# Kernel optimization log

Hardware: AMD Instinct MI355X
Metric: run time of the kernel (lower is better)

## Reference

```python
import jax, jax.numpy as jnp
import numpy as np

N = 50000
E = 800000
IN_DIM = 128
EMB_DIM = 64
HID = 128
OUT_DIM = 64
VOCAB = 1000
NUM_GRAPHS = 128


def _gat(x, src, dst, W, a_s, a_d, b, n):
    # PyG GATConv, heads=1: h = x @ W (no bias); alpha_e = leaky_relu(a_s.h_src + a_d.h_dst, 0.2)
    h = x @ W                                  # [n, C]
    as_n = h @ a_s                             # [n]
    ad_n = h @ a_d                             # [n]
    logit = jax.nn.leaky_relu(as_n[src] + ad_n[dst], negative_slope=0.2)  # [E']
    # segment softmax over destination node
    m = jax.ops.segment_max(logit, dst, num_segments=n)
    e = jnp.exp(logit - m[dst])
    s = jax.ops.segment_sum(e, dst, num_segments=n)
    coef = e / s[dst]                          # [E']
    out = jax.ops.segment_sum(h[src] * coef[:, None], dst, num_segments=n)
    return out + b


def setup_inputs() -> dict:
    key = jax.random.key(0)
    ks = jax.random.split(key, 20)
    inp = {
        "x": jax.random.normal(ks[0], (N, IN_DIM), dtype=jnp.float32),
        "node_index": jax.random.randint(ks[1], (N,), 0, VOCAB),
        "edge_index": jax.random.randint(ks[2], (2, E), 0, N),
        "batch": jnp.sort(jax.random.randint(ks[3], (N,), 0, NUM_GRAPHS)),
        "emb": jax.random.normal(ks[4], (VOCAB, EMB_DIM), dtype=jnp.float32) * 0.1,
        "W1": jax.random.normal(ks[5], (IN_DIM + EMB_DIM, HID), dtype=jnp.float32) * 0.05,
        "a1s": jax.random.normal(ks[6], (HID,), dtype=jnp.float32) * 0.1,
        "a1d": jax.random.normal(ks[7], (HID,), dtype=jnp.float32) * 0.1,
        "b1": jnp.zeros((HID,), dtype=jnp.float32),
        "W2": jax.random.normal(ks[8], (HID, HID), dtype=jnp.float32) * 0.05,
        "a2s": jax.random.normal(ks[9], (HID,), dtype=jnp.float32) * 0.1,
        "a2d": jax.random.normal(ks[10], (HID,), dtype=jnp.float32) * 0.1,
        "b2": jnp.zeros((HID,), dtype=jnp.float32),
        "W3": jax.random.normal(ks[11], (HID, HID), dtype=jnp.float32) * 0.05,
        "a3s": jax.random.normal(ks[12], (HID,), dtype=jnp.float32) * 0.1,
        "a3d": jax.random.normal(ks[13], (HID,), dtype=jnp.float32) * 0.1,
        "b3": jnp.zeros((HID,), dtype=jnp.float32),
        "fcW": jax.random.normal(ks[14], (HID, OUT_DIM), dtype=jnp.float32) * 0.05,
        "fcb": jnp.zeros((OUT_DIM,), dtype=jnp.float32),
    }
    return inp


def reference(x, node_index, edge_index, batch, emb, W1, a1s, a1d, b1,
              W2, a2s, a2d, b2, W3, a3s, a3d, b3, fcW, fcb):
    n = x.shape[0]
    # embedding lookup + L2 normalize features, then concat
    ev = emb[node_index]                       # [N, EMB_DIM]
    norms = jnp.linalg.norm(x, axis=1, keepdims=True)
    norms = jnp.where(norms == 0, 1e-8, norms)
    h = jnp.concatenate([x / norms, ev], axis=1)  # [N, IN+EMB]
    # add self loops (PyG GATConv default add_self_loops=True)
    loop = jnp.arange(n)
    src = jnp.concatenate([edge_index[0], loop])
    dst = jnp.concatenate([edge_index[1], loop])
    h = jax.nn.gelu(_gat(h, src, dst, W1, a1s, a1d, b1, n))
    h = jax.nn.gelu(_gat(h, src, dst, W2, a2s, a2d, b2, n))
    h = jax.nn.gelu(_gat(h, src, dst, W3, a3s, a3d, b3, n))
    # global_add_pool over graphs
    g = jax.ops.segment_sum(h, batch, num_segments=NUM_GRAPHS)  # [G, HID]
    out = g @ fcW + fcb
    return jax.nn.leaky_relu(out, negative_slope=0.01)
```

## Files before the change

kernel.cpp:

```cpp
#include <hip/hip_runtime.h>

#define N_NODES 50000
#define N_EDGES 800000
#define IN_DIM 128
#define EMB_DIM 64
#define HID 128
#define OUT_DIM 64
#define NUM_GRAPHS 128
#define E_TOT (N_EDGES + N_NODES)
#define K1 (IN_DIM + EMB_DIM)
#define BSH 8
#define BNODES 256
#define NB 196
#define EPT 16
#define EPB (256 * EPT)
#define PREPA_BLOCKS 12500
#define BHIST_BLOCKS 512
#define PB_CAP 5376

typedef __attribute__((ext_vector_type(8))) short bf16x8;
typedef __attribute__((ext_vector_type(4))) float f32x4;

__device__ __forceinline__ float gelu_f(float x) {
    float x3 = x * x * x;
    return 0.5f * x * (1.0f + tanhf(0.7978845608028654f * (x + 0.044715f * x3)));
}
__device__ __forceinline__ float lrelu02(float x) { return x > 0.f ? x : 0.2f * x; }
__device__ __forceinline__ unsigned short f2bf(float f) {
    unsigned u = __float_as_uint(f);
    unsigned r = (u + 0x7fffu + ((u >> 16) & 1u)) >> 16;
    return (unsigned short)r;
}
__device__ __forceinline__ unsigned pk2bf(float a, float b) {
    return (unsigned)f2bf(a) | ((unsigned)f2bf(b) << 16);
}

__global__ __launch_bounds__(128) void k_prepW3(const float* __restrict__ W1, unsigned short* __restrict__ Wt1,
                                                const float* __restrict__ W2, unsigned short* __restrict__ Wt2,
                                                const float* __restrict__ W3, unsigned short* __restrict__ Wt3,
                                                int* __restrict__ bcnt, int* __restrict__ bfill) {
    int b = blockIdx.x;
    int c = threadIdx.x;
    if (b == K1 + 2 * HID) {
        for (int i = c; i < NB; i += 128) { bcnt[i] = 0; bfill[i] = 0; }
        return;
    }
    if (b < K1) {
        Wt1[(size_t)c * (K1 + 8) + b] = f2bf(W1[(size_t)b * HID + c]);
    } else if (b < K1 + HID) {
        int k = b - K1;
        Wt2[(size_t)c * (HID + 8) + k] = f2bf(W2[(size_t)k * HID + c]);
    } else {
        int k = b - K1 - HID;
        Wt3[(size_t)c * (HID + 8) + k] = f2bf(W3[(size_t)k * HID + c]);
    }
}

__global__ __launch_bounds__(256) void k_prepA_bhist(const float* __restrict__ x, const int* __restrict__ nidx,
                                                     const float* __restrict__ emb, unsigned* __restrict__ Abu,
                                                     const int* __restrict__ dst, int* __restrict__ bcnt) {
    __shared__ int h[NB];
    if (blockIdx.x >= PREPA_BLOCKS) {
        int nb = blockIdx.x - PREPA_BLOCKS;
        for (int i = threadIdx.x; i < NB; i += 256) h[i] = 0;
        __syncthreads();
        for (int e = nb * 256 + threadIdx.x; e < N_EDGES; e += BHIST_BLOCKS * 256)
            atomicAdd(&h[dst[e] >> BSH], 1);
        __syncthreads();
        for (int i = threadIdx.x; i < NB; i += 256)
            if (h[i]) atomicAdd(&bcnt[i], h[i]);
        return;
    }
    int lane = threadIdx.x & 63;
    int node = (blockIdx.x * 256 + threadIdx.x) >> 6;
    if (node >= N_NODES) return;
    float2 v = ((const float2*)(x + (size_t)node * IN_DIM))[lane];
    float ss = v.x * v.x + v.y * v.y;
#pragma unroll
    for (int o = 32; o; o >>= 1) ss += __shfl_xor(ss, o);
    float nrm = sqrtf(ss);
    if (nrm == 0.f) nrm = 1e-8f;
    float inv = 1.f / nrm;
    unsigned* row = Abu + (size_t)node * (K1 / 2);
    row[lane] = pk2bf(v.x * inv, v.y * inv);
    int nid = __builtin_amdgcn_readfirstlane(nidx[node]);
    if (lane < 32) {
        float2 e = ((const float2*)(emb + (size_t)nid * EMB_DIM))[lane];
        row[64 + lane] = pk2bf(e.x, e.y);
    }
}

__global__ __launch_bounds__(512) void k_bscan(const int* __restrict__ bcnt, int* __restrict__ boff,
                                               int* __restrict__ rowptr) {
    __shared__ int sh[512];
    int t = threadIdx.x;
    int v = (t < NB) ? bcnt[t] : 0;
    sh[t] = v;
    __syncthreads();
    for (int o = 1; o < 512; o <<= 1) {
        int u = (t >= o) ? sh[t - o] : 0;
        __syncthreads();
        sh[t] += u;
        __syncthreads();
    }
    if (t < NB) boff[t] = sh[t] - v;
    if (t == NB - 1) boff[NB] = sh[t];
    if (t == 0) rowptr[N_NODES] = E_TOT;
}

__global__ __launch_bounds__(256) void k_passA(const int* __restrict__ src, const int* __restrict__ dst,
                                               const int* __restrict__ boff, int* __restrict__ bfill,
                                               unsigned* __restrict__ barr) {
    __shared__ int h[NB];
    __shared__ int hbase[NB];
    __shared__ int lofs[NB];
    __shared__ int ssc[256];
    __shared__ unsigned val[EPB];
    __shared__ unsigned char bid[EPB];
    int t = threadIdx.x;
    for (int i = t; i < NB; i += 256) h[i] = 0;
    __syncthreads();
    int e0 = blockIdx.x * EPB;
    int tag[EPT];
#pragma unroll
    for (int i = 0; i < EPT; i++) {
        int e = e0 + i * 256 + t;
        tag[i] = -1;
        if (e < N_EDGES) {
            int b = dst[e] >> BSH;
            int r = atomicAdd(&h[b], 1);
            tag[i] = (b << 12) | r;
        }
    }
    __syncthreads();
    int v = (t < NB) ? h[t] : 0;
    ssc[t] = v;
    __syncthreads();
    for (int o = 1; o < 256; o <<= 1) {
        int u = (t >= o) ? ssc[t - o] : 0;
        __syncthreads();
        ssc[t] += u;
        __syncthreads();
    }
    if (t < NB) {
        lofs[t] = ssc[t] - v;
        hbase[t] = v ? atomicAdd(&bfill[t], v) : 0;
    }
    __syncthreads();
    int tot = ssc[255];
#pragma unroll
    for (int i = 0; i < EPT; i++) {
        if (tag[i] >= 0) {
            int e = e0 + i * 256 + t;
            int b = tag[i] >> 12, r = tag[i] & 0xfff;
            unsigned s = (unsigned)src[e];
            unsigned dl = (unsigned)(dst[e] & (BNODES - 1));
            int idx = lofs[b] + r;
            val[idx] = s | (dl << 16);
            bid[idx] = (unsigned char)b;
        }
    }
    __syncthreads();
    for (int i = t; i < tot; i += 256) {
        int b = bid[i];
        barr[boff[b] + hbase[b] + (i - lofs[b])] = val[i];
    }
}

__global__ __launch_bounds__(256) void k_passB(const unsigned* __restrict__ barr, const int* __restrict__ boff,
                                               int* __restrict__ rowptr, int* __restrict__ csr) {
    __shared__ int dcnt[256];
    __shared__ int dsum[256];
    __shared__ int locOff[256];
    __shared__ unsigned stg[PB_CAP];
    int b = blockIdx.x;
    int t = threadIdx.x;
    int n0 = b << BSH;
    int cnt = min(BNODES, N_NODES - n0);
    int eb = boff[b], ee = boff[b + 1];
    int ne = ee - eb;
    dcnt[t] = 0;
    __syncthreads();
    for (int i = eb + t; i < ee; i += 256) atomicAdd(&dcnt[barr[i] >> 16], 1);
    __syncthreads();
    int v = (t < cnt) ? dcnt[t] + 1 : 0;
    dsum[t] = v;
    __syncthreads();
    for (int o = 1; o < 256; o <<= 1) {
        int u = (t >= o) ? dsum[t - o] : 0;
        __syncthreads();
        dsum[t] += u;
        __syncthreads();
    }
    int csrBase = eb + n0;
    locOff[t] = dsum[t] - v;
    dcnt[t] = 0;
    if (t < cnt) rowptr[n0 + t] = csrBase + locOff[t];
    int total = ne + cnt;
    __syncthreads();
    if (total <= PB_CAP) {
        if (t < cnt) stg[locOff[t]] = (unsigned)(n0 + t);
        for (int i = eb + t; i < ee; i += 256) {
            unsigned vv = barr[i];
            int dl = vv >> 16;
            int k = atomicAdd(&dcnt[dl], 1);
            stg[locOff[dl] + 1 + k] = vv & 0xffffu;
        }
        __syncthreads();
        for (int i = t; i < total; i += 256) csr[csrBase + i] = (int)stg[i];
    } else {
        if (t < cnt) csr[csrBase + locOff[t]] = n0 + t;
        for (int i = eb + t; i < ee; i += 256) {
            unsigned vv = barr[i];
            int dl = vv >> 16;
            int k = atomicAdd(&dcnt[dl], 1);
            csr[csrBase + locOff[dl] + 1 + k] = (int)(vv & 0xffffu);
        }
    }
}

template <int K>
__global__ __launch_bounds__(256) void k_mgemm(const unsigned short* __restrict__ Abf,
                                               const unsigned short* __restrict__ WtP,
                                               const float* __restrict__ a_s, const float* __restrict__ a_d,
                                               unsigned short* __restrict__ Hbf,
                                               float* __restrict__ asn, float* __restrict__ adn) {
    constexpr int KP = K + 8;
    constexpr int NK = K / 32;
    __shared__ __align__(16) unsigned short Wl[128 * KP];
    {
        const uint4* gsrc = (const uint4*)WtP;
        uint4* ldst = (uint4*)Wl;
        const int nchunk = 128 * KP * 2 / 16;
        for (int i = threadIdx.x; i < nchunk; i += 256) ldst[i] = gsrc[i];
    }
    int lane = threadIdx.x & 63;
    int wv = threadIdx.x >> 6;
    int rowbase = blockIdx.x * 64 + wv * 16;
    if (rowbase >= N_NODES) { __syncthreads(); return; }
    int l15 = lane & 15, quad = lane >> 4;

    const unsigned short* Abase = Abf + (size_t)(rowbase + l15) * K + quad * 8;
    bf16x8 afr[NK];
#pragma unroll
    for (int i = 0; i < NK; i++) afr[i] = *(const bf16x8*)(Abase + i * 32);

    __syncthreads();

    f32x4 acc[8];
#pragma unroll
    for (int t = 0; t < 8; t++) acc[t] = (f32x4){0.f, 0.f, 0.f, 0.f};
#pragma unroll
    for (int i = 0; i < NK; i++) {
#pragma unroll
        for (int t = 0; t < 8; t++) {
            bf16x8 bf = *(const bf16x8*)(&Wl[(t * 16 + l15) * KP + i * 32 + quad * 8]);
            acc[t] = __builtin_amdgcn_mfma_f32_16x16x32_bf16(afr[i], bf, acc[t], 0, 0, 0);
        }
    }
    float asc[8], adc[8];
#pragma unroll
    for (int t = 0; t < 8; t++) { asc[t] = a_s[t * 16 + l15]; adc[t] = a_d[t * 16 + l15]; }
#pragma unroll
    for (int r = 0; r < 4; r++) {
        int row = rowbase + quad * 4 + r;
        float ps = 0.f, pd = 0.f;
#pragma unroll
        for (int t = 0; t < 8; t++) {
            float v = acc[t][r];
            Hbf[(size_t)row * HID + t * 16 + l15] = f2bf(v);
            ps = fmaf(v, asc[t], ps);
            pd = fmaf(v, adc[t], pd);
        }
#pragma unroll
        for (int o = 1; o < 16; o <<= 1) {
            ps += __shfl_xor(ps, o);
            pd += __shfl_xor(pd, o);
        }
        if (l15 == 0) { asn[row] = ps; adn[row] = pd; }
    }
}

template <bool OUT32>
__global__ __launch_bounds__(256) void k_aggr(const int* __restrict__ rowptr, const int* __restrict__ csr,
                                              const float* __restrict__ asn, const float* __restrict__ adn,
                                              const unsigned short* __restrict__ hbf,
                                              const float* __restrict__ bias, void* __restrict__ outp) {
    __shared__ float sh_e[4][64];
    __shared__ int sh_s[4][64];
    int lane = threadIdx.x & 63;
    int w = threadIdx.x >> 6;
    int node = blockIdx.x * 4 + w;
    if (node >= N_NODES) return;
    int st = rowptr[node], en = rowptr[node + 1];
    int deg = en - st;
    float ad = adn[node];

    if (deg <= 64) {
        int s = 0;
        float l = -1e30f;
        if (lane < deg) {
            s = csr[st + lane];
            l = lrelu02(asn[s] + ad);
        }
        float m = l;
#pragma unroll
        for (int o = 32; o; o >>= 1) m = fmaxf(m, __shfl_xor(m, o));
        float e = (lane < deg) ? __expf(l - m) : 0.f;
        float ssum = e;
#pragma unroll
        for (int o = 32; o; o >>= 1) ssum += __shfl_xor(ssum, o);
        float coef = e / ssum;

        const uint2* hu2 = (const uint2*)hbf;
        int half = lane >> 5, li = lane & 31;
        float4 acc = make_float4(0.f, 0.f, 0.f, 0.f);
        int j = 0;
        for (; j + 16 <= deg; j += 16) {
            int sx[8];
            float cf[8];
            uint2 vv[8];
#pragma unroll
            for (int q = 0; q < 8; q++) {
                int ii = j + 2 * q + half;
                sx[q] = __shfl(s, ii);
                cf[q] = __shfl(coef, ii);
            }
#pragma unroll
            for (int q = 0; q < 8; q++) vv[q] = hu2[(size_t)sx[q] * 32 + li];
#pragma unroll
            for (int q = 0; q < 8; q++) {
                acc.x = fmaf(cf[q], __int_as_float(vv[q].x << 16), acc.x);
                acc.y = fmaf(cf[q], __int_as_float(vv[q].x & 0xffff0000u), acc.y);
                acc.z = fmaf(cf[q], __int_as_float(vv[q].y << 16), acc.z);
                acc.w = fmaf(cf[q], __int_as_float(vv[q].y & 0xffff0000u), acc.w);
            }
        }
        for (; j + 8 <= deg; j += 8) {
            int sx[4];
            float cf[4];
            uint2 vv[4];
#pragma unroll
            for (int q = 0; q < 4; q++) {
                int ii = j + 2 * q + half;
                sx[q] = __shfl(s, ii);
                cf[q] = __shfl(coef, ii);
            }
#pragma unroll
            for (int q = 0; q < 4; q++) vv[q] = hu2[(size_t)sx[q] * 32 + li];
#pragma unroll
            for (int q = 0; q < 4; q++) {
                acc.x = fmaf(cf[q], __int_as_float(vv[q].x << 16), acc.x);
                acc.y = fmaf(cf[q], __int_as_float(vv[q].x & 0xffff0000u), acc.y);
                acc.z = fmaf(cf[q], __int_as_float(vv[q].y << 16), acc.z);
                acc.w = fmaf(cf[q], __int_as_float(vv[q].y & 0xffff0000u), acc.w);
            }
        }
        for (; j < deg; j += 2) {
            int ii = j + half;
            int ok = ii < deg;
            int ic = ok ? ii : j;
            int sx = __shfl(s, ic);
            float cf = __shfl(coef, ic);
            if (!ok) cf = 0.f;
            uint2 v = hu2[(size_t)sx * 32 + li];
            acc.x = fmaf(cf, __int_as_float(v.x << 16), acc.x);
            acc.y = fmaf(cf, __int_as_float(v.x & 0xffff0000u), acc.y);
            acc.z = fmaf(cf, __int_as_float(v.y << 16), acc.z);
            acc.w = fmaf(cf, __int_as_float(v.y & 0xffff0000u), acc.w);
        }
        acc.x += __shfl_xor(acc.x, 32);
        acc.y += __shfl_xor(acc.y, 32);
        acc.z += __shfl_xor(acc.z, 32);
        acc.w += __shfl_xor(acc.w, 32);
        float4 bb = ((const float4*)bias)[li];
        float r0 = gelu_f(acc.x + bb.x);
        float r1 = gelu_f(acc.y + bb.y);
        float r2 = gelu_f(acc.z + bb.z);
        float r3 = gelu_f(acc.w + bb.w);
        if (half == 0) {
            if constexpr (OUT32) {
                ((float4*)outp)[(size_t)node * 32 + li] = make_float4(r0, r1, r2, r3);
            } else {
                uint2 o;
                o.x = pk2bf(r0, r1);
                o.y = pk2bf(r2, r3);
                ((uint2*)outp)[(size_t)node * 32 + li] = o;
            }
        }
    } else {
        const unsigned* hu = (const unsigned*)hbf;
        float2 acc = make_float2(0.f, 0.f);
        float m = -1e30f;
        for (int i = st + lane; i < en; i += 64) {
            float l = lrelu02(asn[csr[i]] + ad);
            m = fmaxf(m, l);
        }
#pragma unroll
        for (int o = 32; o; o >>= 1) m = fmaxf(m, __shfl_xor(m, o));
        float ssum = 0.f;
        for (int i = st + lane; i < en; i += 64) {
            float l = lrelu02(asn[csr[i]] + ad);
            ssum += __expf(l - m);
        }
#pragma unroll
        for (int o = 32; o; o >>= 1) ssum += __shfl_xor(ssum, o);
        float inv = 1.f / ssum;
        for (int base = st; base < en; base += 64) {
            int cnt = min(64, en - base);
            if (lane < cnt) {
                int sx = csr[base + lane];
                float l = lrelu02(asn[sx] + ad);
                sh_e[w][lane] = __expf(l - m) * inv;
                sh_s[w][lane] = sx;
            }
            for (int j = 0; j < cnt; j++) {
                float c = sh_e[w][j];
                int sx = sh_s[w][j];
                unsigned v0 = hu[(size_t)sx * 64 + lane];
                acc.x = fmaf(c, __int_as_float(v0 << 16), acc.x);
                acc.y = fmaf(c, __int_as_float(v0 & 0xffff0000u), acc.y);
            }
        }
        float2 b = ((const float2*)bias)[lane];
        float rx = gelu_f(acc.x + b.x);
        float ry = gelu_f(acc.y + b.y);
        if constexpr (OUT32) {
            ((float2*)outp)[(size_t)node * 64 + lane] = make_float2(rx, ry);
        } else {
            ((unsigned*)outp)[(size_t)node * 64 + lane] = pk2bf(rx, ry);
        }
    }
}

__global__ __launch_bounds__(256) void k_poolfc(const float* __restrict__ h, const int* __restrict__ batch,
                                                const float* __restrict__ fcW, const float* __restrict__ fcb,
                                                float* __restrict__ out) {
    __shared__ float gv[HID];
    __shared__ float tmp[256];
    int g = blockIdx.x;
    int st, en;
    {
        int lo = 0, hi = N_NODES;
        while (lo < hi) { int mid = (lo + hi) >> 1; if (batch[mid] < g) lo = mid + 1; else hi = mid; }
        st = lo;
        lo = st; hi = N_NODES;
        while (lo < hi) { int mid = (lo + hi) >> 1; if (batch[mid] < g + 1) lo = mid + 1; else hi = mid; }
        en = lo;
    }
    int c = threadIdx.x & 127;
    int half = threadIdx.x >> 7;
    float acc = 0.f;
#pragma unroll 4
    for (int n = st + half; n < en; n += 2) acc += h[(size_t)n * HID + c];
    tmp[threadIdx.x] = acc;
    __syncthreads();
    if (threadIdx.x < HID) gv[threadIdx.x] = tmp[threadIdx.x] + tmp[threadIdx.x + 128];
    __syncthreads();
    if (threadIdx.x < OUT_DIM) {
        float a = fcb[threadIdx.x];
#pragma unroll 4
        for (int k = 0; k < HID; k++) a = fmaf(gv[k], fcW[k * OUT_DIM + threadIdx.x], a);
        out[g * OUT_DIM + threadIdx.x] = a > 0.f ? a : 0.01f * a;
    }
}

extern "C" void kernel_launch(void* const* d_in, const int* in_sizes, int n_in,
                              void* d_out, int out_size, void* d_ws, size_t ws_size,
                              hipStream_t stream) {
    const float* x    = (const float*)d_in[0];
    const int* nidx   = (const int*)d_in[1];
    const int* ei     = (const int*)d_in[2];
    const int* batch  = (const int*)d_in[3];
    const float* emb  = (const float*)d_in[4];
    const float* W1   = (const float*)d_in[5];
    const float* a1s  = (const float*)d_in[6];
    const float* a1d  = (const float*)d_in[7];
    const float* b1   = (const float*)d_in[8];
    const float* W2   = (const float*)d_in[9];
    const float* a2s  = (const float*)d_in[10];
    const float* a2d  = (const float*)d_in[11];
    const float* b2   = (const float*)d_in[12];
    const float* W3   = (const float*)d_in[13];
    const float* a3s  = (const float*)d_in[14];
    const float* a3d  = (const float*)d_in[15];
    const float* b3   = (const float*)d_in[16];
    const float* fcW  = (const float*)d_in[17];
    const float* fcb  = (const float*)d_in[18];
    float* out = (float*)d_out;
    const int* srcA = ei;
    const int* dstA = ei + N_EDGES;

    char* w = (char*)d_ws;
    auto alloc = [&](size_t bytes) -> char* {
        char* p = w;
        w += (bytes + 511) & ~(size_t)511;
        return p;
    };
    char* region0 = alloc((size_t)N_NODES * HID * 4);
    unsigned* Abu = (unsigned*)region0;
    float* h3f    = (float*)region0;
    unsigned short* hLin = (unsigned short*)alloc((size_t)N_NODES * HID * 2);
    unsigned short* hAct = (unsigned short*)alloc((size_t)N_NODES * HID * 2);
    float* asn   = (float*)alloc((size_t)N_NODES * 4);
    float* adn   = (float*)alloc((size_t)N_NODES * 4);
    int* rowptr  = (int*)alloc((size_t)(N_NODES + 1) * 4);
    int* bcnt    = (int*)alloc((size_t)NB * 4);
    int* boff    = (int*)alloc((size_t)(NB + 1) * 4);
    int* bfill   = (int*)alloc((size_t)NB * 4);
    unsigned* barr = (unsigned*)alloc((size_t)N_EDGES * 4);
    int* csr     = (int*)alloc((size_t)E_TOT * 4);
    unsigned short* Wt1 = (unsigned short*)alloc((size_t)HID * (K1 + 8) * 2);
    unsigned short* Wt2 = (unsigned short*)alloc((size_t)HID * (HID + 8) * 2);
    unsigned short* Wt3 = (unsigned short*)alloc((size_t)HID * (HID + 8) * 2);

    k_prepW3<<<K1 + 2 * HID + 1, 128, 0, stream>>>(W1, Wt1, W2, Wt2, W3, Wt3, bcnt, bfill);
    k_prepA_bhist<<<PREPA_BLOCKS + BHIST_BLOCKS, 256, 0, stream>>>(x, nidx, emb, Abu, dstA, bcnt);

    k_bscan<<<1, 512, 0, stream>>>(bcnt, boff, rowptr);
    k_passA<<<(N_EDGES + EPB - 1) / EPB, 256, 0, stream>>>(srcA, dstA, boff, bfill, barr);
    k_passB<<<NB, 256, 0, stream>>>(barr, boff, rowptr, csr);

    int gemmBlocks = (N_NODES + 63) / 64;
    int aggrBlocks = (N_NODES + 3) / 4;

    k_mgemm<K1><<<gemmBlocks, 256, 0, stream>>>((const unsigned short*)Abu, Wt1, a1s, a1d, hLin, asn, adn);
    k_aggr<false><<<aggrBlocks, 256, 0, stream>>>(rowptr, csr, asn, adn, hLin, b1, hAct);
    k_mgemm<HID><<<gemmBlocks, 256, 0, stream>>>(hAct, Wt2, a2s, a2d, hLin, asn, adn);
    k_aggr<false><<<aggrBlocks, 256, 0, stream>>>(rowptr, csr, asn, adn, hLin, b2, hAct);
    k_mgemm<HID><<<gemmBlocks, 256, 0, stream>>>(hAct, Wt3, a3s, a3d, hLin, asn, adn);
    k_aggr<true><<<aggrBlocks, 256, 0, stream>>>(rowptr, csr, asn, adn, hLin, b3, h3f);

    k_poolfc<<<NUM_GRAPHS, 256, 0, stream>>>(h3f, batch, fcW, fcb, out);
}
```

Measured before the change: 339.7 us.

## Fold bucket scan into passA, drop LDS W staging, simplify aggregation gather

Removes the single-block k_bscan launch by having every passA block recompute the bucket prefix scan redundantly, with block 0 writing boff and passB writing the rowptr sentinel. The GEMM now reads weight fragments directly from global memory/cache instead of staging them in LDS with a barrier. The low-degree aggregation path switches from half-wave uint2 gathers via shuffles to full-wave 32-bit gathers using readlane, sharing the epilogue with the high-degree path. Pooling uses 512 threads per graph. The risks are fewer bytes per gather load, more total loads, and uncached global weight reads in the GEMM.

```diff
diff --git a/kernel.cpp b/kernel.cpp
--- a/kernel.cpp
+++ b/kernel.cpp
@@ -26,6 +26,9 @@
     return 0.5f * x * (1.0f + tanhf(0.7978845608028654f * (x + 0.044715f * x3)));
 }
 __device__ __forceinline__ float lrelu02(float x) { return x > 0.f ? x : 0.2f * x; }
+__device__ __forceinline__ float rl_f(float v, int j) {
+    return __int_as_float(__builtin_amdgcn_readlane(__float_as_int(v), j));
+}
 __device__ __forceinline__ unsigned short f2bf(float f) {
     unsigned u = __float_as_uint(f);
     unsigned r = (u + 0x7fffu + ((u >> 16) & 1u)) >> 16;
@@ -74,6 +77,7 @@
     int lane = threadIdx.x & 63;
     int node = (blockIdx.x * 256 + threadIdx.x) >> 6;
     if (node >= N_NODES) return;
+    int nid = nidx[node];
     float2 v = ((const float2*)(x + (size_t)node * IN_DIM))[lane];
     float ss = v.x * v.x + v.y * v.y;
 #pragma unroll
@@ -83,42 +87,39 @@
     float inv = 1.f / nrm;
     unsigned* row = Abu + (size_t)node * (K1 / 2);
     row[lane] = pk2bf(v.x * inv, v.y * inv);
-    int nid = __builtin_amdgcn_readfirstlane(nidx[node]);
+    nid = __builtin_amdgcn_readfirstlane(nid);
     if (lane < 32) {
         float2 e = ((const float2*)(emb + (size_t)nid * EMB_DIM))[lane];
         row[64 + lane] = pk2bf(e.x, e.y);
     }
 }
 
-__global__ __launch_bounds__(512) void k_bscan(const int* __restrict__ bcnt, int* __restrict__ boff,
-                                               int* __restrict__ rowptr) {
-    __shared__ int sh[512];
-    int t = threadIdx.x;
-    int v = (t < NB) ? bcnt[t] : 0;
-    sh[t] = v;
-    __syncthreads();
-    for (int o = 1; o < 512; o <<= 1) {
-        int u = (t >= o) ? sh[t - o] : 0;
-        __syncthreads();
-        sh[t] += u;
-        __syncthreads();
-    }
-    if (t < NB) boff[t] = sh[t] - v;
-    if (t == NB - 1) boff[NB] = sh[t];
-    if (t == 0) rowptr[N_NODES] = E_TOT;
-}
-
 __global__ __launch_bounds__(256) void k_passA(const int* __restrict__ src, const int* __restrict__ dst,
-                                               const int* __restrict__ boff, int* __restrict__ bfill,
-                                               unsigned* __restrict__ barr) {
+                                               const int* __restrict__ bcnt, int* __restrict__ boff,
+                                               int* __restrict__ bfill, unsigned* __restrict__ barr) {
     __shared__ int h[NB];
     __shared__ int hbase[NB];
     __shared__ int lofs[NB];
+    __shared__ int gbo[NB];
     __shared__ int ssc[256];
     __shared__ unsigned val[EPB];
     __shared__ unsigned char bid[EPB];
     int t = threadIdx.x;
     for (int i = t; i < NB; i += 256) h[i] = 0;
+    int gv = (t < NB) ? bcnt[t] : 0;
+    ssc[t] = gv;
+    __syncthreads();
+    for (int o = 1; o < 256; o <<= 1) {
+        int u = (t >= o) ? ssc[t - o] : 0;
+        __syncthreads();
+        ssc[t] += u;
+        __syncthreads();
+    }
+    if (t < NB) gbo[t] = ssc[t] - gv;
+    if (blockIdx.x == 0) {
+        if (t < NB) boff[t] = ssc[t] - gv;
+        if (t == NB - 1) boff[NB] = ssc[t];
+    }
     __syncthreads();
     int e0 = blockIdx.x * EPB;
     int tag[EPT];
@@ -163,7 +164,7 @@
     __syncthreads();
     for (int i = t; i < tot; i += 256) {
         int b = bid[i];
-        barr[boff[b] + hbase[b] + (i - lofs[b])] = val[i];
+        barr[gbo[b] + hbase[b] + (i - lofs[b])] = val[i];
     }
 }
 
@@ -175,6 +176,7 @@
     __shared__ unsigned stg[PB_CAP];
     int b = blockIdx.x;
     int t = threadIdx.x;
+    if (b == 0 && t == 0) rowptr[N_NODES] = E_TOT;
     int n0 = b << BSH;
     int cnt = min(BNODES, N_NODES - n0);
     int eb = boff[b], ee = boff[b + 1];
@@ -227,17 +229,10 @@
                                                float* __restrict__ asn, float* __restrict__ adn) {
     constexpr int KP = K + 8;
     constexpr int NK = K / 32;
-    __shared__ __align__(16) unsigned short Wl[128 * KP];
-    {
-        const uint4* gsrc = (const uint4*)WtP;
-        uint4* ldst = (uint4*)Wl;
-        const int nchunk = 128 * KP * 2 / 16;
-        for (int i = threadIdx.x; i < nchunk; i += 256) ldst[i] = gsrc[i];
-    }
     int lane = threadIdx.x & 63;
     int wv = threadIdx.x >> 6;
     int rowbase = blockIdx.x * 64 + wv * 16;
-    if (rowbase >= N_NODES) { __syncthreads(); return; }
+    if (rowbase >= N_NODES) return;
     int l15 = lane & 15, quad = lane >> 4;
 
     const unsigned short* Abase = Abf + (size_t)(rowbase + l15) * K + quad * 8;
@@ -245,8 +240,7 @@
 #pragma unroll
     for (int i = 0; i < NK; i++) afr[i] = *(const bf16x8*)(Abase + i * 32);
 
-    __syncthreads();
-
+    const unsigned short* Wb = WtP + (size_t)l15 * KP + quad * 8;
     f32x4 acc[8];
 #pragma unroll
     for (int t = 0; t < 8; t++) acc[t] = (f32x4){0.f, 0.f, 0.f, 0.f};
@@ -254,7 +248,7 @@
     for (int i = 0; i < NK; i++) {
 #pragma unroll
         for (int t = 0; t < 8; t++) {
-            bf16x8 bf = *(const bf16x8*)(&Wl[(t * 16 + l15) * KP + i * 32 + quad * 8]);
+            bf16x8 bf = *(const bf16x8*)(Wb + (size_t)t * 16 * KP + i * 32);
             acc[t] = __builtin_amdgcn_mfma_f32_16x16x32_bf16(afr[i], bf, acc[t], 0, 0, 0);
         }
     }
@@ -295,6 +289,8 @@
     int st = rowptr[node], en = rowptr[node + 1];
     int deg = en - st;
     float ad = adn[node];
+    const unsigned* hu = (const unsigned*)hbf;
+    float2 acc = make_float2(0.f, 0.f);
 
     if (deg <= 64) {
         int s = 0;
@@ -311,86 +307,52 @@
 #pragma unroll
         for (int o = 32; o; o >>= 1) ssum += __shfl_xor(ssum, o);
         float coef = e / ssum;
-
-        const uint2* hu2 = (const uint2*)hbf;
-        int half = lane >> 5, li = lane & 31;
-        float4 acc = make_float4(0.f, 0.f, 0.f, 0.f);
         int j = 0;
-        for (; j + 16 <= deg; j += 16) {
-            int sx[8];
-            float cf[8];
-            uint2 vv[8];
+        for (; j + 8 <= deg; j += 8) {
+            int si[8];
+            float ci[8];
+            unsigned vi[8];
 #pragma unroll
             for (int q = 0; q < 8; q++) {
-                int ii = j + 2 * q + half;
-                sx[q] = __shfl(s, ii);
-                cf[q] = __shfl(coef, ii);
+                si[q] = __builtin_amdgcn_readlane(s, j + q);
+                ci[q] = rl_f(coef, j + q);
             }
 #pragma unroll
-            for (int q = 0; q < 8; q++) vv[q] = hu2[(size_t)sx[q] * 32 + li];
+            for (int q = 0; q < 8; q++) vi[q] = hu[(size_t)si[q] * 64 + lane];
 #pragma unroll
             for (int q = 0; q < 8; q++) {
-                acc.x = fmaf(cf[q], __int_as_float(vv[q].x << 16), acc.x);
-                acc.y = fmaf(cf[q], __int_as_float(vv[q].x & 0xffff0000u), acc.y);
-                acc.z = fmaf(cf[q], __int_as_float(vv[q].y << 16), acc.z);
-                acc.w = fmaf(cf[q], __int_as_float(vv[q].y & 0xffff0000u), acc.w);
+                acc.x = fmaf(ci[q], __int_as_float(vi[q] << 16), acc.x);
+                acc.y = fmaf(ci[q], __int_as_float(vi[q] & 0xffff0000u), acc.y);
             }
         }
-        for (; j + 8 <= deg; j += 8) {
-            int sx[4];
-            float cf[4];
-            uint2 vv[4];
-#pragma unroll
-            for (int q = 0; q < 4; q++) {
-                int ii = j + 2 * q + half;
-                sx[q] = __shfl(s, ii);
-                cf[q] = __shfl(coef, ii);
-            }
-#pragma unroll
-            for (int q = 0; q < 4; q++) vv[q] = hu2[(size_t)sx[q] * 32 + li];
-#pragma unroll
-            for (int q = 0; q < 4; q++) {
-                acc.x = fmaf(cf[q], __int_as_float(vv[q].x << 16), acc.x);
-                acc.y = fmaf(cf[q], __int_as_float(vv[q].x & 0xffff0000u), acc.y);
-                acc.z = fmaf(cf[q], __int_as_float(vv[q].y << 16), acc.z);
-                acc.w = fmaf(cf[q], __int_as_float(vv[q].y & 0xffff0000u), acc.w);
-            }
-        }
-        for (; j < deg; j += 2) {
-            int ii = j + half;
-            int ok = ii < deg;
-            int ic = ok ? ii : j;
-            int sx = __shfl(s, ic);
-            float cf = __shfl(coef, ic);
-            if (!ok) cf = 0.f;
-            uint2 v = hu2[(size_t)sx * 32 + li];
-            acc.x = fmaf(cf, __int_as_float(v.x << 16), acc.x);
-            acc.y = fmaf(cf, __int_as_float(v.x & 0xffff0000u), acc.y);
-            acc.z = fmaf(cf, __int_as_float(v.y << 16), acc.z);
-            acc.w = fmaf(cf, __int_as_float(v.y & 0xffff0000u), acc.w);
-        }
-        acc.x += __shfl_xor(acc.x, 32);
-        acc.y += __shfl_xor(acc.y, 32);
-        acc.z += __shfl_xor(acc.z, 32);
-        acc.w += __shfl_xor(acc.w, 32);
-        float4 bb = ((const float4*)bias)[li];
-        float r0 = gelu_f(acc.x + bb.x);
-        float r1 = gelu_f(acc.y + bb.y);
-        float r2 = gelu_f(acc.z + bb.z);
-        float r3 = gelu_f(acc.w + bb.w);
-        if (half == 0) {
-            if constexpr (OUT32) {
-                ((float4*)outp)[(size_t)node * 32 + li] = make_float4(r0, r1, r2, r3);
-            } else {
-                uint2 o;
-                o.x = pk2bf(r0, r1);
-                o.y = pk2bf(r2, r3);
-                ((uint2*)outp)[(size_t)node * 32 + li] = o;
-            }
+        for (; j + 4 <= deg; j += 4) {
+            int s0 = __builtin_amdgcn_readlane(s, j);
+            int s1 = __builtin_amdgcn_readlane(s, j + 1);
+            int s2 = __builtin_amdgcn_readlane(s, j + 2);
+            int s3 = __builtin_amdgcn_readlane(s, j + 3);
+            float c0 = rl_f(coef, j), c1 = rl_f(coef, j + 1);
+            float c2 = rl_f(coef, j + 2), c3 = rl_f(coef, j + 3);
+            unsigned v0 = hu[(size_t)s0 * 64 + lane];
+            unsigned v1 = hu[(size_t)s1 * 64 + lane];
+            unsigned v2 = hu[(size_t)s2 * 64 + lane];
+            unsigned v3 = hu[(size_t)s3 * 64 + lane];
+            acc.x = fmaf(c0, __int_as_float(v0 << 16), acc.x);
+            acc.y = fmaf(c0, __int_as_float(v0 & 0xffff0000u), acc.y);
+            acc.x = fmaf(c1, __int_as_float(v1 << 16), acc.x);
+            acc.y = fmaf(c1, __int_as_float(v1 & 0xffff0000u), acc.y);
+            acc.x = fmaf(c2, __int_as_float(v2 << 16), acc.x);
+            acc.y = fmaf(c2, __int_as_float(v2 & 0xffff0000u), acc.y);
+            acc.x = fmaf(c3, __int_as_float(v3 << 16), acc.x);
+            acc.y = fmaf(c3, __int_as_float(v3 & 0xffff0000u), acc.y);
+        }
+        for (; j < deg; j++) {
+            int s0 = __builtin_amdgcn_readlane(s, j);
+            float c0 = rl_f(coef, j);
+            unsigned v0 = hu[(size_t)s0 * 64 + lane];
+            acc.x = fmaf(c0, __int_as_float(v0 << 16), acc.x);
+            acc.y = fmaf(c0, __int_as_float(v0 & 0xffff0000u), acc.y);
         }
     } else {
-        const unsigned* hu = (const unsigned*)hbf;
-        float2 acc = make_float2(0.f, 0.f);
         float m = -1e30f;
         for (int i = st + lane; i < en; i += 64) {
             float l = lrelu02(asn[csr[i]] + ad);
@@ -422,22 +384,22 @@
                 acc.y = fmaf(c, __int_as_float(v0 & 0xffff0000u), acc.y);
             }
         }
-        float2 b = ((const float2*)bias)[lane];
-        float rx = gelu_f(acc.x + b.x);
-        float ry = gelu_f(acc.y + b.y);
-        if constexpr (OUT32) {
-            ((float2*)outp)[(size_t)node * 64 + lane] = make_float2(rx, ry);
-        } else {
-            ((unsigned*)outp)[(size_t)node * 64 + lane] = pk2bf(rx, ry);
-        }
-    }
-}
-
-__global__ __launch_bounds__(256) void k_poolfc(const float* __restrict__ h, const int* __restrict__ batch,
+    }
+    float2 b = ((const float2*)bias)[lane];
+    float rx = gelu_f(acc.x + b.x);
+    float ry = gelu_f(acc.y + b.y);
+    if constexpr (OUT32) {
+        ((float2*)outp)[(size_t)node * 64 + lane] = make_float2(rx, ry);
+    } else {
+        ((unsigned*)outp)[(size_t)node * 64 + lane] = pk2bf(rx, ry);
+    }
+}
+
+__global__ __launch_bounds__(512) void k_poolfc(const float* __restrict__ h, const int* __restrict__ batch,
                                                 const float* __restrict__ fcW, const float* __restrict__ fcb,
                                                 float* __restrict__ out) {
     __shared__ float gv[HID];
-    __shared__ float tmp[256];
+    __shared__ float tmp[512];
     int g = blockIdx.x;
     int st, en;
     {
@@ -449,13 +411,14 @@
         en = lo;
     }
     int c = threadIdx.x & 127;
-    int half = threadIdx.x >> 7;
+    int part = threadIdx.x >> 7;
     float acc = 0.f;
 #pragma unroll 4
-    for (int n = st + half; n < en; n += 2) acc += h[(size_t)n * HID + c];
+    for (int n = st + part; n < en; n += 4) acc += h[(size_t)n * HID + c];
     tmp[threadIdx.x] = acc;
     __syncthreads();
-    if (threadIdx.x < HID) gv[threadIdx.x] = tmp[threadIdx.x] + tmp[threadIdx.x + 128];
+    if (threadIdx.x < HID)
+        gv[threadIdx.x] = tmp[threadIdx.x] + tmp[threadIdx.x + 128] + tmp[threadIdx.x + 256] + tmp[threadIdx.x + 384];
     __syncthreads();
     if (threadIdx.x < OUT_DIM) {
         float a = fcb[threadIdx.x];
@@ -517,8 +480,7 @@
     k_prepW3<<<K1 + 2 * HID + 1, 128, 0, stream>>>(W1, Wt1, W2, Wt2, W3, Wt3, bcnt, bfill);
     k_prepA_bhist<<<PREPA_BLOCKS + BHIST_BLOCKS, 256, 0, stream>>>(x, nidx, emb, Abu, dstA, bcnt);
 
-    k_bscan<<<1, 512, 0, stream>>>(bcnt, boff, rowptr);
-    k_passA<<<(N_EDGES + EPB - 1) / EPB, 256, 0, stream>>>(srcA, dstA, boff, bfill, barr);
+    k_passA<<<(N_EDGES + EPB - 1) / EPB, 256, 0, stream>>>(srcA, dstA, bcnt, boff, bfill, barr);
     k_passB<<<NB, 256, 0, stream>>>(barr, boff, rowptr, csr);
 
     int gemmBlocks = (N_NODES + 63) / 64;
@@ -531,5 +493,5 @@
     k_mgemm<HID><<<gemmBlocks, 256, 0, stream>>>(hAct, Wt3, a3s, a3d, hLin, asn, adn);
     k_aggr<true><<<aggrBlocks, 256, 0, stream>>>(rowptr, csr, asn, adn, hLin, b3, h3f);
 
-    k_poolfc<<<NUM_GRAPHS, 256, 0, stream>>>(h3f, batch, fcW, fcb, out);
-}
+    k_poolfc<<<NUM_GRAPHS, 512, 0, stream>>>(h3f, batch, fcW, fcb, out);
+}
```

Measured after the change: 331.7 us. -2.3%, faster.
